# Optimization experiments

Hardware: AMD Instinct MI355X
Metric: run time of the kernel (lower is better)

## Reference

```python
import jax, jax.numpy as jnp
import numpy as np

B, N, T, FD = 128, 64, 20, 2
E, H, A = 16, 32, 32
DB, DH = 30.0, 30.0
NB, NHD = 12, 12  # 360/30 bearing and heading bins
DOMAIN_INIT = 5.0
EPS = 1e-12


def setup_inputs() -> dict:
    key = jax.random.key(0)
    ks = jax.random.split(key, 20)
    rn = lambda k, s, sc=0.1: (jax.random.normal(k, s) * sc).astype(jnp.float32)
    return {
        'x': jax.random.normal(ks[0], (B, N, T, FD), jnp.float32),
        'dmat': jax.random.uniform(ks[1], (B, N, T, N), jnp.float32) * 10.0,
        'bmat': jax.random.uniform(ks[2], (B, N, T, N), jnp.float32) * 360.0,
        'hmat': jax.random.uniform(ks[3], (B, N, T, N), jnp.float32) * 360.0,
        'mask': jnp.ones((B, N, T), jnp.float32),
        'emb_W': rn(ks[4], (E, FD)), 'emb_b': rn(ks[5], (E,)),
        'W_ih': rn(ks[6], (4 * H, E)), 'W_hh': rn(ks[7], (4 * H, H)),
        'b_ih': rn(ks[8], (4 * H,)), 'b_hh': rn(ks[9], (4 * H,)),
        'domain': jnp.full((NB, NHD), DOMAIN_INIT, jnp.float32),
        'enc2att_W': rn(ks[10], (A, H)), 'enc2att_b': rn(ks[11], (A,)),
        'spa_W': rn(ks[12], (A, 2 * A)), 'spa_b': rn(ks[13], (A,)),
        'att2enc_W': rn(ks[14], (H, A)), 'att2enc_b': rn(ks[15], (H,)),
        'cls_W': rn(ks[16], (1, H)), 'cls_b': rn(ks[17], (1,)),
        'h0': jax.random.normal(ks[18], (B * N, H), jnp.float32),
        'c0': jax.random.normal(ks[19], (B * N, H), jnp.float32),
    }


def _forward(x, dmat, bmat, hmat, mask, emb_W, emb_b, W_ih, W_hh, b_ih, b_hh,
             domain, enc2att_W, enc2att_b, spa_W, spa_b, att2enc_W, att2enc_b,
             cls_W, cls_b, h0, c0):
    # input embedding: [B,N,T,F] -> [T, B*N, E] (time-major for scan)
    xe = jnp.einsum('bntf,ef->bnte', x, emb_W) + emb_b
    xe = jnp.moveaxis(xe.reshape(B * N, T, E), 1, 0)
    dm_t = jnp.moveaxis(dmat, 2, 0)   # [T,B,N,N]
    bm_t = jnp.moveaxis(bmat, 2, 0)
    hm_t = jnp.moveaxis(hmat, 2, 0)
    mk_t = jnp.moveaxis(mask, 2, 0)   # [T,B,N]
    eye = jnp.eye(N, dtype=x.dtype)

    def step(carry, inputs):
        h, c = carry                     # [B*N, H]
        xt, dm, bm, hm, mk = inputs
        # single-step LSTM cell (torch gate order i,f,g,o)
        g = xt @ W_ih.T + b_ih + h @ W_hh.T + b_hh
        i, f, gg, o = jnp.split(g, 4, axis=-1)
        c = jax.nn.sigmoid(f) * c + jax.nn.sigmoid(i) * jnp.tanh(gg)
        h = jax.nn.sigmoid(o) * jnp.tanh(c)
        # project encoder state to attention space: [B,N,A]
        a = h.reshape(B, N, H) @ enc2att_W.T + enc2att_b
        # spatial attention weights from distance/bearing/heading edge feats
        ib = jnp.clip(jnp.floor(bm / DB), 0, NB - 1).astype(jnp.int32)
        ih = jnp.clip(jnp.floor(hm / DH), 0, NHD - 1).astype(jnp.int32)
        w = jax.nn.relu(domain[ib, ih] - dm)               # [B,N,N]
        w = w * mk[:, :, None] * mk[:, None, :] * (1.0 - eye)
        w = w / (jnp.sum(w, axis=-1, keepdims=True) + EPS)
        att = jnp.einsum('bij,bjd->bid', w, a)
        z = jnp.tanh(jnp.concatenate([a, att], axis=-1) @ spa_W.T + spa_b)
        h = (z @ att2enc_W.T + att2enc_b).reshape(B * N, H)
        return (h, c), None

    (h, c), _ = jax.lax.scan(step, (h0, c0), (xe, dm_t, bm_t, hm_t, mk_t))
    scores = jnp.tanh(h.reshape(B, N, H) @ cls_W.T + cls_b)
    return jax.nn.sigmoid(scores)  # [B, N, 1]


def reference(x, dmat, bmat, hmat, mask, emb_W, emb_b, W_ih, W_hh, b_ih, b_hh,
              domain, enc2att_W, enc2att_b, spa_W, spa_b, att2enc_W, att2enc_b,
              cls_W, cls_b, h0, c0):
    return _forward(x, dmat, bmat, hmat, mask, emb_W, emb_b, W_ih, W_hh, b_ih,
                    b_hh, domain, enc2att_W, enc2att_b, spa_W, spa_b,
                    att2enc_W, att2enc_b, cls_W, cls_b, h0, c0)
```

## Files before the change

### kernel.cpp

```cpp
#include <hip/hip_runtime.h>
#include <math.h>

#define T_STEPS 20

typedef _Float16 half8 __attribute__((ext_vector_type(8)));
typedef _Float16 half4v __attribute__((ext_vector_type(4)));
typedef float f32x4 __attribute__((ext_vector_type(4)));

__device__ __forceinline__ float sigm(float v) {
  return __builtin_amdgcn_rcpf(1.0f + __expf(-v));
}
__device__ __forceinline__ float tanh_f(float v) {
  return 1.0f - 2.0f * __builtin_amdgcn_rcpf(1.0f + __expf(2.0f * v));
}

__device__ __forceinline__ void barrier_lgkm() {
  asm volatile("s_waitcnt lgkmcnt(0)" ::: "memory");
  __builtin_amdgcn_s_barrier();
  asm volatile("" ::: "memory");
}

__global__ __launch_bounds__(1024)
void traj_disc(const float* __restrict__ x, const float* __restrict__ dmat,
               const float* __restrict__ bmat, const float* __restrict__ hmat,
               const float* __restrict__ maskp,
               const float* __restrict__ embW, const float* __restrict__ embb,
               const float* __restrict__ Wih, const float* __restrict__ Whh,
               const float* __restrict__ bih, const float* __restrict__ bhh,
               const float* __restrict__ dom,
               const float* __restrict__ e2aW, const float* __restrict__ e2ab,
               const float* __restrict__ spaW, const float* __restrict__ spab,
               const float* __restrict__ a2eW, const float* __restrict__ a2eb,
               const float* __restrict__ clsW, const float* __restrict__ clsb,
               const float* __restrict__ h0p, const float* __restrict__ c0p,
               float* __restrict__ out)
{
  __shared__ __align__(16) _Float16 sgw[128*40];
  __shared__ __align__(16) _Float16 sgwc[128*40];
  __shared__ __align__(16) float4   sgmb[128];
  __shared__ __align__(16) _Float16 sESaT[32*40];
  __shared__ __align__(16) _Float16 sEStT[32*40];
  __shared__ float bz[32];
  __shared__ float sdom[144];
  __shared__ float sm[1280];
  __shared__ float sclsc[32];
  __shared__ float sclsb2[1];
  __shared__ __align__(16) _Float16 sH[64*40];
  __shared__ __align__(16) _Float16 sw[64*72];
  __shared__ __align__(16) _Float16 sz_[64*40];
  __shared__ __align__(16) _Float16 sQT[32*72];
  __shared__ __align__(16) float sgates[128*68];

  const int tid = threadIdx.x;
  const int b = blockIdx.x;
  const int i = tid >> 4;
  const int s = tid & 15;
  const int w = tid >> 6;
  const int l = tid & 63;
  const int quad = l >> 4;
  const int n16 = l & 15;

  for (int idx = tid; idx < 4096; idx += 1024) sgw[(idx >> 5)*40 + (idx & 31)] = (_Float16)Whh[idx];
  {
    const int g = tid >> 3, kb = (tid & 7) << 2;
    float a0 = 0.f, a1 = 0.f, a2 = 0.f, a3 = 0.f;
    #pragma unroll
    for (int h = 0; h < 32; ++h) {
      const float wv = Whh[g*32 + h];
      a0 = fmaf(wv, a2eW[h*32 + kb + 0], a0);
      a1 = fmaf(wv, a2eW[h*32 + kb + 1], a1);
      a2 = fmaf(wv, a2eW[h*32 + kb + 2], a2);
      a3 = fmaf(wv, a2eW[h*32 + kb + 3], a3);
    }
    sgwc[g*40 + kb + 0] = (_Float16)a0; sgwc[g*40 + kb + 1] = (_Float16)a1;
    sgwc[g*40 + kb + 2] = (_Float16)a2; sgwc[g*40 + kb + 3] = (_Float16)a3;
  }
  if (tid < 128) {
    float m0 = 0.f, m1 = 0.f, b0 = bih[tid] + bhh[tid];
    #pragma unroll
    for (int e = 0; e < 16; ++e) {
      float wv_ = Wih[tid*16 + e];
      m0 = fmaf(wv_, embW[2*e],   m0);
      m1 = fmaf(wv_, embW[2*e+1], m1);
      b0 = fmaf(wv_, embb[e],     b0);
    }
    float bn = b0;
    #pragma unroll
    for (int h = 0; h < 32; ++h) bn = fmaf(Whh[tid*32 + h], a2eb[h], bn);
    sgmb[tid] = make_float4(m0, m1, b0, bn);
  }
  {
    const int zk = tid >> 5, hc = tid & 31;
    float sa_ = 0.f, st_ = 0.f;
    #pragma unroll
    for (int a = 0; a < 32; ++a) {
      const float ev = e2aW[a*32 + hc];
      sa_ = fmaf(spaW[zk*64 + a],      ev, sa_);
      st_ = fmaf(spaW[zk*64 + 32 + a], ev, st_);
    }
    sESaT[zk*40 + hc] = (_Float16)sa_;
    sEStT[zk*40 + hc] = (_Float16)st_;
  }
  if (tid < 32) {
    float acc = spab[tid];
    #pragma unroll
    for (int a = 0; a < 32; ++a)
      acc = fmaf(e2ab[a], spaW[tid*64 + a] + spaW[tid*64 + 32 + a], acc);
    bz[tid] = acc;
    float cc = 0.f;
    #pragma unroll
    for (int h = 0; h < 32; ++h) cc = fmaf(clsW[h], a2eW[h*32 + tid], cc);
    sclsc[tid] = cc;
  }
  if (tid == 0) {
    float cb = clsb[0];
    #pragma unroll
    for (int h = 0; h < 32; ++h) cb = fmaf(clsW[h], a2eb[h], cb);
    sclsb2[0] = cb;
  }
  if (tid < 144) sdom[tid] = dom[tid];
  for (int idx = tid; idx < 1280; idx += 1024) sm[idx] = maskp[(size_t)b*1280 + idx];
  for (int idx = tid; idx < 2048; idx += 1024) sH[(idx >> 5)*40 + (idx & 31)] = (_Float16)h0p[(size_t)b*2048 + idx];
  float c0r = c0p[(size_t)b*2048 + i*32 + s];
  float c1r = c0p[(size_t)b*2048 + i*32 + s + 16];
  __syncthreads();

  const size_t nb = (size_t)b*64 + i;

  const float* xpre = x + (size_t)(b*64 + ((w >> 2) << 4) + (quad << 2)) * 40;
  float2 xA = *(const float2*)(xpre +   0);
  float2 xB = *(const float2*)(xpre +  40);
  float2 xC = *(const float2*)(xpre +  80);
  float2 xD = *(const float2*)(xpre + 120);
  size_t eb_ = nb*1280;
  float dm0 = dmat[eb_ + s],      bm0 = bmat[eb_ + s],      hm0 = hmat[eb_ + s];
  float dm1 = dmat[eb_ + s + 16], bm1 = bmat[eb_ + s + 16], hm1 = hmat[eb_ + s + 16];
  float dm2 = dmat[eb_ + s + 32], bm2 = bmat[eb_ + s + 32], hm2 = hmat[eb_ + s + 32];
  float dm3 = dmat[eb_ + s + 48], bm3 = bmat[eb_ + s + 48], hm3 = hmat[eb_ + s + 48];

  #pragma unroll 1
  for (int t = 0; t < T_STEPS; ++t) {
    {
      const int r1 = w >> 2, cp = (w & 3) << 1;
      const _Float16* Abase = (t == 0) ? sH : sz_;
      const _Float16* Bbase = (t == 0) ? sgw : sgwc;
      const half8 Af = *(const half8*)(Abase + (16*r1 + n16)*40 + quad*8);
#define OP1C(c) { \
      const half8 Bf = *(const half8*)(Bbase + (16*(c) + n16)*40 + quad*8); \
      const float4 mb = sgmb[16*(c) + n16]; \
      const float bb = (t == 0) ? mb.z : mb.w; \
      f32x4 Cv; \
      Cv[0] = fmaf(xA.x, mb.x, fmaf(xA.y, mb.y, bb)); \
      Cv[1] = fmaf(xB.x, mb.x, fmaf(xB.y, mb.y, bb)); \
      Cv[2] = fmaf(xC.x, mb.x, fmaf(xC.y, mb.y, bb)); \
      Cv[3] = fmaf(xD.x, mb.x, fmaf(xD.y, mb.y, bb)); \
      Cv = __builtin_amdgcn_mfma_f32_16x16x32_f16(Af, Bf, Cv, 0, 0, 0); \
      *(f32x4*)(sgates + (16*(c) + n16)*68 + 16*r1 + 4*quad) = Cv; }
      OP1C(cp) OP1C(cp + 1)
#undef OP1C
    }
    barrier_lgkm();

    {
#define GR(q, u) sgates[((q)*32 + s + 16*(u))*68 + i]
      const float ai0 = GR(0,0), af0 = GR(1,0), ag0 = GR(2,0), ao0 = GR(3,0);
      const float ai1 = GR(0,1), af1 = GR(1,1), ag1 = GR(2,1), ao1 = GR(3,1);
#undef GR
      c0r = fmaf(sigm(af0), c0r, sigm(ai0)*tanh_f(ag0));
      sH[i*40 + s]      = (_Float16)(sigm(ao0)*tanh_f(c0r));
      c1r = fmaf(sigm(af1), c1r, sigm(ai1)*tanh_f(ag1));
      sH[i*40 + s + 16] = (_Float16)(sigm(ao1)*tanh_f(c1r));
    }
    {
      const float mi_ = sm[i*20 + t];
      float rs = 0.0f;
#define WCOMP(jj) float wn##jj; { \
      int ib_ = (int)floorf(bm##jj * (1.0f/30.0f)); ib_ = ib_ < 0 ? 0 : (ib_ > 11 ? 11 : ib_); \
      int ih_ = (int)floorf(hm##jj * (1.0f/30.0f)); ih_ = ih_ < 0 ? 0 : (ih_ > 11 ? 11 : ih_); \
      float w_ = fmaxf(sdom[ib_*12 + ih_] - dm##jj, 0.0f) * (mi_ * sm[(s + 16*(jj))*20 + t]); \
      wn##jj = (s + 16*(jj) == i) ? 0.0f : w_; rs += wn##jj; }
      WCOMP(0) WCOMP(1) WCOMP(2) WCOMP(3)
#undef WCOMP
      rs += __shfl_xor(rs, 1); rs += __shfl_xor(rs, 2);
      rs += __shfl_xor(rs, 4); rs += __shfl_xor(rs, 8);
      const float inv_ = __builtin_amdgcn_rcpf(rs + 1e-12f);
      sw[i*72 + s +  0] = (_Float16)(wn0 * inv_);
      sw[i*72 + s + 16] = (_Float16)(wn1 * inv_);
      sw[i*72 + s + 32] = (_Float16)(wn2 * inv_);
      sw[i*72 + s + 48] = (_Float16)(wn3 * inv_);
    }
    {
      const int tn = (t < T_STEPS - 1) ? t + 1 : t;
      const size_t ebn = (nb*20 + tn)*64;
      dm0 = dmat[ebn + s];      bm0 = bmat[ebn + s];      hm0 = hmat[ebn + s];
      dm1 = dmat[ebn + s + 16]; bm1 = bmat[ebn + s + 16]; hm1 = hmat[ebn + s + 16];
      dm2 = dmat[ebn + s + 32]; bm2 = bmat[ebn + s + 32]; hm2 = hmat[ebn + s + 32];
      dm3 = dmat[ebn + s + 48]; bm3 = bmat[ebn + s + 48]; hm3 = hmat[ebn + s + 48];
      const int tn2 = tn << 1;
      xA = *(const float2*)(xpre + tn2);
      xB = *(const float2*)(xpre + tn2 +  40);
      xC = *(const float2*)(xpre + tn2 +  80);
      xD = *(const float2*)(xpre + tn2 + 120);
    }
    barrier_lgkm();

    f32x4 Pv = {0.f, 0.f, 0.f, 0.f};
    if (w < 8) {
      const int r = w >> 1, c = w & 1;
      const half8 Af = *(const half8*)(sH    + (16*r + n16)*40 + quad*8);
      const half8 Bf = *(const half8*)(sESaT + (16*c + n16)*40 + quad*8);
      const float bzv = bz[16*c + n16];
      Pv[0] = bzv; Pv[1] = bzv; Pv[2] = bzv; Pv[3] = bzv;
      Pv = __builtin_amdgcn_mfma_f32_16x16x32_f16(Af, Bf, Pv, 0, 0, 0);
    } else {
      const int w8 = w - 8, r = w8 >> 1, c = w8 & 1;
      const half8 Af = *(const half8*)(sH    + (16*r + n16)*40 + quad*8);
      const half8 Bf = *(const half8*)(sEStT + (16*c + n16)*40 + quad*8);
      f32x4 Cv = {0.f, 0.f, 0.f, 0.f};
      Cv = __builtin_amdgcn_mfma_f32_16x16x32_f16(Af, Bf, Cv, 0, 0, 0);
      half4v hq;
      hq[0] = (_Float16)Cv[0]; hq[1] = (_Float16)Cv[1];
      hq[2] = (_Float16)Cv[2]; hq[3] = (_Float16)Cv[3];
      *(half4v*)(sQT + (16*c + n16)*72 + 16*r + 4*quad) = hq;
    }
    barrier_lgkm();

    if (w < 8) {
      const int r = w >> 1, c = w & 1;
      const half8 A0 = *(const half8*)(sw  + (16*r + n16)*72 + quad*8);
      const half8 A1 = *(const half8*)(sw  + (16*r + n16)*72 + 32 + quad*8);
      const half8 B0 = *(const half8*)(sQT + (16*c + n16)*72 + quad*8);
      const half8 B1 = *(const half8*)(sQT + (16*c + n16)*72 + 32 + quad*8);
      Pv = __builtin_amdgcn_mfma_f32_16x16x32_f16(A0, B0, Pv, 0, 0, 0);
      Pv = __builtin_amdgcn_mfma_f32_16x16x32_f16(A1, B1, Pv, 0, 0, 0);
      const int nd = 16*r + 4*quad;
      sz_[(nd+0)*40 + 16*c + n16] = (_Float16)tanh_f(Pv[0]);
      sz_[(nd+1)*40 + 16*c + n16] = (_Float16)tanh_f(Pv[1]);
      sz_[(nd+2)*40 + 16*c + n16] = (_Float16)tanh_f(Pv[2]);
      sz_[(nd+3)*40 + 16*c + n16] = (_Float16)tanh_f(Pv[3]);
    }
    barrier_lgkm();
  }

  if (tid < 64) {
    float acc = sclsb2[0];
    #pragma unroll
    for (int k = 0; k < 32; ++k) acc = fmaf((float)sz_[tid*40 + k], sclsc[k], acc);
    out[(size_t)b*64 + tid] = sigm(tanh_f(acc));
  }
}

extern "C" void kernel_launch(void* const* d_in, const int* in_sizes, int n_in,
                              void* d_out, int out_size, void* d_ws, size_t ws_size,
                              hipStream_t stream) {
  (void)in_sizes; (void)n_in; (void)d_ws; (void)ws_size; (void)out_size;
  const float* x    = (const float*)d_in[0];
  const float* dmat = (const float*)d_in[1];
  const float* bmat = (const float*)d_in[2];
  const float* hmat = (const float*)d_in[3];
  const float* mask = (const float*)d_in[4];
  const float* embW = (const float*)d_in[5];
  const float* embb = (const float*)d_in[6];
  const float* Wih  = (const float*)d_in[7];
  const float* Whh  = (const float*)d_in[8];
  const float* bih  = (const float*)d_in[9];
  const float* bhh  = (const float*)d_in[10];
  const float* dom  = (const float*)d_in[11];
  const float* e2aW = (const float*)d_in[12];
  const float* e2ab = (const float*)d_in[13];
  const float* spaW = (const float*)d_in[14];
  const float* spab = (const float*)d_in[15];
  const float* a2eW = (const float*)d_in[16];
  const float* a2eb = (const float*)d_in[17];
  const float* clsW = (const float*)d_in[18];
  const float* clsb = (const float*)d_in[19];
  const float* h0   = (const float*)d_in[20];
  const float* c0   = (const float*)d_in[21];
  float* out = (float*)d_out;

  traj_disc<<<dim3(128), dim3(1024), 0, stream>>>(
      x, dmat, bmat, hmat, mask, embW, embb, Wih, Whh, bih, bhh, dom,
      e2aW, e2ab, spaW, spab, a2eW, a2eb, clsW, clsb, h0, c0, out);
}
```

Before: 223.2 us.

## Split LSTM gates and edge weights across wave halves, keep gates in registers

The gate MFMA work moves to waves 0-7, and each wave now computes all four gates for its tile, so the LSTM cell update runs straight from the MFMA accumulators. This removes the sgates shared buffer and one barrier per step. Waves 8-15 compute the attention edge weights at the same time, using vectorised float4 loads of dmat, bmat and hmat and packed half8 stores. In exchange, each gate wave issues more MFMAs in sequence, and only half the block's waves do each task.

```diff
diff --git a/kernel.cpp b/kernel.cpp
--- a/kernel.cpp
+++ b/kernel.cpp
@@ -49,12 +49,9 @@
   __shared__ __align__(16) _Float16 sw[64*72];
   __shared__ __align__(16) _Float16 sz_[64*40];
   __shared__ __align__(16) _Float16 sQT[32*72];
-  __shared__ __align__(16) float sgates[128*68];
 
   const int tid = threadIdx.x;
   const int b = blockIdx.x;
-  const int i = tid >> 4;
-  const int s = tid & 15;
   const int w = tid >> 6;
   const int l = tid & 63;
   const int quad = l >> 4;
@@ -120,87 +117,93 @@
   }
   if (tid < 144) sdom[tid] = dom[tid];
   for (int idx = tid; idx < 1280; idx += 1024) sm[idx] = maskp[(size_t)b*1280 + idx];
-  for (int idx = tid; idx < 2048; idx += 1024) sH[(idx >> 5)*40 + (idx & 31)] = (_Float16)h0p[(size_t)b*2048 + idx];
-  float c0r = c0p[(size_t)b*2048 + i*32 + s];
-  float c1r = c0p[(size_t)b*2048 + i*32 + s + 16];
+  for (int idx = tid; idx < 2048; idx += 1024) sz_[(idx >> 5)*40 + (idx & 31)] = (_Float16)h0p[(size_t)b*2048 + idx];
+
+  f32x4 ccell;
+  float2 xA, xB, xC, xD;
+  f32x4 dmv0, dmv1, bmv0, bmv1, hmv0, hmv1;
+  const float* xpre = nullptr;
+  size_t ebp = 0;
+  if (w < 8) {
+    const int rr = w >> 1, uu = w & 1;
+    const int hh = 16*uu + n16;
+    #pragma unroll
+    for (int reg = 0; reg < 4; ++reg)
+      ccell[reg] = c0p[(size_t)b*2048 + (size_t)(16*rr + 4*quad + reg)*32 + hh];
+    xpre = x + (size_t)(b*64 + 16*rr + 4*quad) * 40;
+    xA = *(const float2*)(xpre +   0);
+    xB = *(const float2*)(xpre +  40);
+    xC = *(const float2*)(xpre +  80);
+    xD = *(const float2*)(xpre + 120);
+  } else {
+    const int i8 = (tid - 512) >> 3, s8 = tid & 7;
+    ebp = ((size_t)(b*64 + i8)*20)*64 + (size_t)(s8*8);
+    dmv0 = *(const f32x4*)(dmat + ebp); dmv1 = *(const f32x4*)(dmat + ebp + 4);
+    bmv0 = *(const f32x4*)(bmat + ebp); bmv1 = *(const f32x4*)(bmat + ebp + 4);
+    hmv0 = *(const f32x4*)(hmat + ebp); hmv1 = *(const f32x4*)(hmat + ebp + 4);
+  }
   __syncthreads();
-
-  const size_t nb = (size_t)b*64 + i;
-
-  const float* xpre = x + (size_t)(b*64 + ((w >> 2) << 4) + (quad << 2)) * 40;
-  float2 xA = *(const float2*)(xpre +   0);
-  float2 xB = *(const float2*)(xpre +  40);
-  float2 xC = *(const float2*)(xpre +  80);
-  float2 xD = *(const float2*)(xpre + 120);
-  size_t eb_ = nb*1280;
-  float dm0 = dmat[eb_ + s],      bm0 = bmat[eb_ + s],      hm0 = hmat[eb_ + s];
-  float dm1 = dmat[eb_ + s + 16], bm1 = bmat[eb_ + s + 16], hm1 = hmat[eb_ + s + 16];
-  float dm2 = dmat[eb_ + s + 32], bm2 = bmat[eb_ + s + 32], hm2 = hmat[eb_ + s + 32];
-  float dm3 = dmat[eb_ + s + 48], bm3 = bmat[eb_ + s + 48], hm3 = hmat[eb_ + s + 48];
 
   #pragma unroll 1
   for (int t = 0; t < T_STEPS; ++t) {
-    {
-      const int r1 = w >> 2, cp = (w & 3) << 1;
-      const _Float16* Abase = (t == 0) ? sH : sz_;
+    if (w < 8) {
+      const int rr = w >> 1, uu = w & 1;
       const _Float16* Bbase = (t == 0) ? sgw : sgwc;
-      const half8 Af = *(const half8*)(Abase + (16*r1 + n16)*40 + quad*8);
-#define OP1C(c) { \
-      const half8 Bf = *(const half8*)(Bbase + (16*(c) + n16)*40 + quad*8); \
-      const float4 mb = sgmb[16*(c) + n16]; \
+      const half8 Af = *(const half8*)(sz_ + (16*rr + n16)*40 + quad*8);
+      f32x4 G0, G1, G2, G3;
+#define OP1Q(Gq, q) { \
+      const int c_ = 2*(q) + uu; \
+      const half8 Bf = *(const half8*)(Bbase + (16*c_ + n16)*40 + quad*8); \
+      const float4 mb = sgmb[16*c_ + n16]; \
       const float bb = (t == 0) ? mb.z : mb.w; \
       f32x4 Cv; \
       Cv[0] = fmaf(xA.x, mb.x, fmaf(xA.y, mb.y, bb)); \
       Cv[1] = fmaf(xB.x, mb.x, fmaf(xB.y, mb.y, bb)); \
       Cv[2] = fmaf(xC.x, mb.x, fmaf(xC.y, mb.y, bb)); \
       Cv[3] = fmaf(xD.x, mb.x, fmaf(xD.y, mb.y, bb)); \
-      Cv = __builtin_amdgcn_mfma_f32_16x16x32_f16(Af, Bf, Cv, 0, 0, 0); \
-      *(f32x4*)(sgates + (16*(c) + n16)*68 + 16*r1 + 4*quad) = Cv; }
-      OP1C(cp) OP1C(cp + 1)
-#undef OP1C
-    }
-    barrier_lgkm();
-
-    {
-#define GR(q, u) sgates[((q)*32 + s + 16*(u))*68 + i]
-      const float ai0 = GR(0,0), af0 = GR(1,0), ag0 = GR(2,0), ao0 = GR(3,0);
-      const float ai1 = GR(0,1), af1 = GR(1,1), ag1 = GR(2,1), ao1 = GR(3,1);
-#undef GR
-      c0r = fmaf(sigm(af0), c0r, sigm(ai0)*tanh_f(ag0));
-      sH[i*40 + s]      = (_Float16)(sigm(ao0)*tanh_f(c0r));
-      c1r = fmaf(sigm(af1), c1r, sigm(ai1)*tanh_f(ag1));
-      sH[i*40 + s + 16] = (_Float16)(sigm(ao1)*tanh_f(c1r));
-    }
-    {
-      const float mi_ = sm[i*20 + t];
-      float rs = 0.0f;
-#define WCOMP(jj) float wn##jj; { \
-      int ib_ = (int)floorf(bm##jj * (1.0f/30.0f)); ib_ = ib_ < 0 ? 0 : (ib_ > 11 ? 11 : ib_); \
-      int ih_ = (int)floorf(hm##jj * (1.0f/30.0f)); ih_ = ih_ < 0 ? 0 : (ih_ > 11 ? 11 : ih_); \
-      float w_ = fmaxf(sdom[ib_*12 + ih_] - dm##jj, 0.0f) * (mi_ * sm[(s + 16*(jj))*20 + t]); \
-      wn##jj = (s + 16*(jj) == i) ? 0.0f : w_; rs += wn##jj; }
-      WCOMP(0) WCOMP(1) WCOMP(2) WCOMP(3)
-#undef WCOMP
-      rs += __shfl_xor(rs, 1); rs += __shfl_xor(rs, 2);
-      rs += __shfl_xor(rs, 4); rs += __shfl_xor(rs, 8);
-      const float inv_ = __builtin_amdgcn_rcpf(rs + 1e-12f);
-      sw[i*72 + s +  0] = (_Float16)(wn0 * inv_);
-      sw[i*72 + s + 16] = (_Float16)(wn1 * inv_);
-      sw[i*72 + s + 32] = (_Float16)(wn2 * inv_);
-      sw[i*72 + s + 48] = (_Float16)(wn3 * inv_);
-    }
-    {
-      const int tn = (t < T_STEPS - 1) ? t + 1 : t;
-      const size_t ebn = (nb*20 + tn)*64;
-      dm0 = dmat[ebn + s];      bm0 = bmat[ebn + s];      hm0 = hmat[ebn + s];
-      dm1 = dmat[ebn + s + 16]; bm1 = bmat[ebn + s + 16]; hm1 = hmat[ebn + s + 16];
-      dm2 = dmat[ebn + s + 32]; bm2 = bmat[ebn + s + 32]; hm2 = hmat[ebn + s + 32];
-      dm3 = dmat[ebn + s + 48]; bm3 = bmat[ebn + s + 48]; hm3 = hmat[ebn + s + 48];
-      const int tn2 = tn << 1;
+      Gq = __builtin_amdgcn_mfma_f32_16x16x32_f16(Af, Bf, Cv, 0, 0, 0); }
+      OP1Q(G0, 0) OP1Q(G1, 1) OP1Q(G2, 2) OP1Q(G3, 3)
+#undef OP1Q
+      const int hh = 16*uu + n16;
+      #pragma unroll
+      for (int reg = 0; reg < 4; ++reg) {
+        const float cc = fmaf(sigm(G1[reg]), ccell[reg], sigm(G0[reg]) * tanh_f(G2[reg]));
+        ccell[reg] = cc;
+        sH[(16*rr + 4*quad + reg)*40 + hh] = (_Float16)(sigm(G3[reg]) * tanh_f(cc));
+      }
+      const int tn2 = ((t < T_STEPS - 1) ? t + 1 : t) << 1;
       xA = *(const float2*)(xpre + tn2);
       xB = *(const float2*)(xpre + tn2 +  40);
       xC = *(const float2*)(xpre + tn2 +  80);
       xD = *(const float2*)(xpre + tn2 + 120);
+    } else {
+      const int i8 = (tid - 512) >> 3, s8 = tid & 7;
+      const float mi_ = sm[i8*20 + t];
+      f32x4 wnA, wnB;
+      float rs = 0.0f;
+#define WC(dst, k, dmv, bmv, hmv, jof) { \
+      int ib_ = (int)floorf(bmv[k] * (1.0f/30.0f)); ib_ = ib_ < 0 ? 0 : (ib_ > 11 ? 11 : ib_); \
+      int ih_ = (int)floorf(hmv[k] * (1.0f/30.0f)); ih_ = ih_ < 0 ? 0 : (ih_ > 11 ? 11 : ih_); \
+      float w_ = fmaxf(sdom[ib_*12 + ih_] - dmv[k], 0.0f) * (mi_ * sm[(8*s8 + (jof))*20 + t]); \
+      w_ = (8*s8 + (jof) == i8) ? 0.0f : w_; dst[k] = w_; rs += w_; }
+      WC(wnA,0,dmv0,bmv0,hmv0,0) WC(wnA,1,dmv0,bmv0,hmv0,1)
+      WC(wnA,2,dmv0,bmv0,hmv0,2) WC(wnA,3,dmv0,bmv0,hmv0,3)
+      WC(wnB,0,dmv1,bmv1,hmv1,4) WC(wnB,1,dmv1,bmv1,hmv1,5)
+      WC(wnB,2,dmv1,bmv1,hmv1,6) WC(wnB,3,dmv1,bmv1,hmv1,7)
+#undef WC
+      rs += __shfl_xor(rs, 1); rs += __shfl_xor(rs, 2); rs += __shfl_xor(rs, 4);
+      const float inv_ = __builtin_amdgcn_rcpf(rs + 1e-12f);
+      half8 hw;
+      hw[0] = (_Float16)(wnA[0]*inv_); hw[1] = (_Float16)(wnA[1]*inv_);
+      hw[2] = (_Float16)(wnA[2]*inv_); hw[3] = (_Float16)(wnA[3]*inv_);
+      hw[4] = (_Float16)(wnB[0]*inv_); hw[5] = (_Float16)(wnB[1]*inv_);
+      hw[6] = (_Float16)(wnB[2]*inv_); hw[7] = (_Float16)(wnB[3]*inv_);
+      *(half8*)(sw + i8*72 + s8*8) = hw;
+      const int tn = (t < T_STEPS - 1) ? t + 1 : t;
+      const size_t eb2 = ebp + (size_t)tn*64;
+      dmv0 = *(const f32x4*)(dmat + eb2); dmv1 = *(const f32x4*)(dmat + eb2 + 4);
+      bmv0 = *(const f32x4*)(bmat + eb2); bmv1 = *(const f32x4*)(bmat + eb2 + 4);
+      hmv0 = *(const f32x4*)(hmat + eb2); hmv1 = *(const f32x4*)(hmat + eb2 + 4);
     }
     barrier_lgkm();
 
```

New measurement: 206.4 us. -7.6%, faster.
